# Kernel tuning notes

Hardware: AMD Instinct MI355X
Metric: run time of the kernel (lower is better)

## Reference

```python
import jax, jax.numpy as jnp
import numpy as np


def setup_inputs() -> dict:
    key = jax.random.key(0)
    R = 200  # num_regions (Schaefer-200 atlas scale)
    init_state = 0.1 * jax.random.normal(key, (R, 6), dtype=jnp.float32)
    # canonical Jansen-Rit parameters
    params = dict(A=3.25, a=100.0, B=22.0, b=50.0,
                  c1=135.0, c2=0.8 * 135.0, c3=0.25 * 135.0, c4=0.25 * 135.0,
                  vmax=5.0, v0=6.0, r=0.56, std_in=150.0)
    inp = {"init_state": init_state,
           "step_size": jnp.float32(1e-4),
           "num_steps": 20000}
    for k, v in params.items():
        inp[k] = jnp.float32(v)
    return inp


def reference(init_state, step_size, A, a, B, b, c1, c2, c3, c4,
              vmax, v0, r, std_in, num_steps):
    # sigmoid(x) = vmax / (1 + exp(r*(v0 - x)))
    def sig(x):
        return vmax / (1.0 + jnp.exp(r * (v0 - x)))

    dt = step_size

    def step(carry, _):
        M, E, I, Mv, Ev, Iv = carry  # each [R]
        dMv = A * a * sig(E - I) - 2.0 * a * Mv - M * a ** 2
        dEv = A * a * (std_in + c2 * sig(c1 * M)) - 2.0 * a * Ev - E * a ** 2
        dIv = B * b * (c4 * sig(c3 * M)) - 2.0 * b * Iv - I * b ** 2
        new = (M + dt * Mv, E + dt * Ev, I + dt * Iv,
               Mv + dt * dMv, Ev + dt * dEv, Iv + dt * dIv)
        return new, jnp.stack(new, axis=1)  # [R, 6] per-step history

    init = tuple(init_state[:, i] for i in range(6))
    final, state_hist = jax.lax.scan(step, init, None, length=num_steps)
    state_vals = jnp.stack(final, axis=1)  # [R, 6]
    return state_vals, state_hist  # ([R,6], [num_steps, R, 6])
```

## Files before the change

kernel.cpp:

```cpp
#include <hip/hip_runtime.h>


#define RLOG2E 1.44269504088896340736f

__global__ __launch_bounds__(64)
void jansen_kernel(const float* __restrict__ init_state,
                   const float* __restrict__ p_dt,
                   const int*   __restrict__ p_nsteps,
                   const float* __restrict__ pA,    const float* __restrict__ pa,
                   const float* __restrict__ pB,    const float* __restrict__ pb,
                   const float* __restrict__ pc1,   const float* __restrict__ pc2,
                   const float* __restrict__ pc3,   const float* __restrict__ pc4,
                   const float* __restrict__ pvmax, const float* __restrict__ pv0,
                   const float* __restrict__ pr,    const float* __restrict__ pstd,
                   float* __restrict__ out, int R)
{
    const int reg = blockIdx.x * 64 + threadIdx.x;
    if (reg >= R) return;

    const float dt     = *p_dt;
    const int   nsteps = *p_nsteps;
    const float A = *pA, a = *pa, B = *pB, b = *pb;
    const float c1 = *pc1, c2 = *pc2, c3 = *pc3, c4 = *pc4;
    const float vmax = *pvmax, v0 = *pv0, rsl = *pr, std_in = *pstd;

    const float cl2 = rsl * RLOG2E;
    const float cv0 = cl2 * v0;
    const float nE  = -cl2;
    const float nM1 = -cl2 * c1;
    const float nM3 = -cl2 * c3;

    const float kMv = 1.0f - 2.0f * a * dt;
    const float kIv = 1.0f - 2.0f * b * dt;
    const float kM  = -dt * a * a;
    const float kI  = -dt * b * b;
    const float kSE  = dt * A * a * vmax;
    const float kSM1 = dt * A * a * c2 * vmax;
    const float kSM3 = dt * B * b * c4 * vmax;
    const float kIn  = dt * A * a * std_in;

    float M  = init_state[reg * 6 + 0];
    float E  = init_state[reg * 6 + 1];
    float I  = init_state[reg * 6 + 2];
    float Mv = init_state[reg * 6 + 3];
    float Ev = init_state[reg * 6 + 4];
    float Iv = init_state[reg * 6 + 5];

    const int R6 = R * 6;
    float* hist = out + R6 + (size_t)reg * 6;

    #define STEP()                                                              \
    do {                                                                        \
        float eE  = __builtin_amdgcn_exp2f(fmaf(nE,  E - I, cv0));              \
        float eM1 = __builtin_amdgcn_exp2f(fmaf(nM1, M,     cv0));              \
        float eM3 = __builtin_amdgcn_exp2f(fmaf(nM3, M,     cv0));              \
        float rE  = __builtin_amdgcn_rcpf(1.0f + eE);                           \
        float rM1 = __builtin_amdgcn_rcpf(1.0f + eM1);                          \
        float rM3 = __builtin_amdgcn_rcpf(1.0f + eM3);                          \
        float nMv_ = fmaf(kMv, Mv, fmaf(kSE,  rE,  kM * M));                    \
        float nEv_ = fmaf(kMv, Ev, fmaf(kSM1, rM1, fmaf(kM, E, kIn)));          \
        float nIv_ = fmaf(kIv, Iv, fmaf(kSM3, rM3, kI * I));                    \
        float nM_  = fmaf(dt, Mv, M);                                           \
        float nE_  = fmaf(dt, Ev, E);                                           \
        float nI_  = fmaf(dt, Iv, I);                                           \
        M = nM_; E = nE_; I = nI_; Mv = nMv_; Ev = nEv_; Iv = nIv_;             \
        ((float2*)hist)[0] = make_float2(M, E);                                 \
        ((float2*)hist)[1] = make_float2(I, Mv);                                \
        ((float2*)hist)[2] = make_float2(Ev, Iv);                               \
        hist += R6;                                                             \
    } while (0)

    const int UN = 16;
    int s = 0;
    for (; s + UN <= nsteps; s += UN) {
        #pragma unroll
        for (int u = 0; u < UN; ++u) {
            STEP();
        }
    }
    for (; s < nsteps; ++s) {
        STEP();
    }
    #undef STEP

    float* fin = out + reg * 6;
    ((float2*)fin)[0] = make_float2(M, E);
    ((float2*)fin)[1] = make_float2(I, Mv);
    ((float2*)fin)[2] = make_float2(Ev, Iv);
}

extern "C" void kernel_launch(void* const* d_in, const int* in_sizes, int n_in,
                              void* d_out, int out_size, void* d_ws, size_t ws_size,
                              hipStream_t stream)
{
    const float* init = (const float*)d_in[0];
    const float* dt   = (const float*)d_in[1];
    const int*   ns   = (const int*)d_in[2];
    const int R = in_sizes[0] / 6;

    dim3 grid((R + 63) / 64), block(64);
    jansen_kernel<<<grid, block, 0, stream>>>(
        init, dt, ns,
        (const float*)d_in[3],  (const float*)d_in[4],
        (const float*)d_in[5],  (const float*)d_in[6],
        (const float*)d_in[7],  (const float*)d_in[8],
        (const float*)d_in[9],  (const float*)d_in[10],
        (const float*)d_in[11], (const float*)d_in[12],
        (const float*)d_in[13], (const float*)d_in[14],
        (float*)d_out, R);
}
```

Before: 1.474 ms.

## Stage per-step history in LDS and write coalesced chunks to global

Each thread now writes its state for 16 steps into shared memory, and after a barrier the whole block copies those rows to global memory in coalesced float2 writes. The old code issued strided per-thread writes with a 24-byte stride. The aim is to cut the cost of inefficient global store transactions on the 20000-step serial recurrence. In exchange it adds two barriers per chunk plus extra LDS traffic on the latency-bound serial path.

```diff
diff --git a/kernel.cpp b/kernel.cpp
--- a/kernel.cpp
+++ b/kernel.cpp
@@ -2,6 +2,7 @@
 
 
 #define RLOG2E 1.44269504088896340736f
+#define KC 16
 
 __global__ __launch_bounds__(64)
 void jansen_kernel(const float* __restrict__ init_state,
@@ -15,8 +16,12 @@
                    const float* __restrict__ pr,    const float* __restrict__ pstd,
                    float* __restrict__ out, int R)
 {
-    const int reg = blockIdx.x * 64 + threadIdx.x;
-    if (reg >= R) return;
+    __shared__ float lds[KC * 64 * 6];
+
+    const int lane = threadIdx.x;
+    const int blk  = blockIdx.x;
+    const int reg  = blk * 64 + lane;
+    const int lreg = (reg < R) ? reg : (R - 1);
 
     const float dt     = *p_dt;
     const int   nsteps = *p_nsteps;
@@ -39,17 +44,19 @@
     const float kSM3 = dt * B * b * c4 * vmax;
     const float kIn  = dt * A * a * std_in;
 
-    float M  = init_state[reg * 6 + 0];
-    float E  = init_state[reg * 6 + 1];
-    float I  = init_state[reg * 6 + 2];
-    float Mv = init_state[reg * 6 + 3];
-    float Ev = init_state[reg * 6 + 4];
-    float Iv = init_state[reg * 6 + 5];
+    float M  = init_state[lreg * 6 + 0];
+    float E  = init_state[lreg * 6 + 1];
+    float I  = init_state[lreg * 6 + 2];
+    float Mv = init_state[lreg * 6 + 3];
+    float Ev = init_state[lreg * 6 + 4];
+    float Iv = init_state[lreg * 6 + 5];
 
-    const int R6 = R * 6;
-    float* hist = out + R6 + (size_t)reg * 6;
+    const int R6   = R * 6;
+    const int nact = min(64, R - blk * 64);
+    const int S    = nact * 6;
+    float* rowBase = out + R6 + (size_t)blk * 64 * 6;
 
-    #define STEP()                                                              \
+    #define STEP(u)                                                             \
     do {                                                                        \
         float eE  = __builtin_amdgcn_exp2f(fmaf(nE,  E - I, cv0));              \
         float eM1 = __builtin_amdgcn_exp2f(fmaf(nM1, M,     cv0));              \
@@ -64,29 +71,65 @@
         float nE_  = fmaf(dt, Ev, E);                                           \
         float nI_  = fmaf(dt, Iv, I);                                           \
         M = nM_; E = nE_; I = nI_; Mv = nMv_; Ev = nEv_; Iv = nIv_;             \
-        ((float2*)hist)[0] = make_float2(M, E);                                 \
-        ((float2*)hist)[1] = make_float2(I, Mv);                                \
-        ((float2*)hist)[2] = make_float2(Ev, Iv);                               \
-        hist += R6;                                                             \
+        float* l = lds + (u) * 384 + lane * 6;                                  \
+        ((float2*)l)[0] = make_float2(M, E);                                    \
+        ((float2*)l)[1] = make_float2(I, Mv);                                   \
+        ((float2*)l)[2] = make_float2(Ev, Iv);                                  \
     } while (0)
 
-    const int UN = 16;
-    int s = 0;
-    for (; s + UN <= nsteps; s += UN) {
+    const int nchunks = nsteps / KC;
+    for (int c = 0; c < nchunks; ++c) {
         #pragma unroll
-        for (int u = 0; u < UN; ++u) {
-            STEP();
+        for (int u = 0; u < KC; ++u) {
+            STEP(u);
         }
+        __syncthreads();
+
+        float* rb = rowBase + (size_t)(c * KC) * R6;
+        if (S == 384) {
+            #pragma unroll
+            for (int u = 0; u < KC; ++u) {
+                const float* l = lds + u * 384;
+                float*       g = rb + (size_t)u * R6;
+                #pragma unroll
+                for (int p = 0; p < 3; ++p) {
+                    int d = p * 128 + 2 * lane;
+                    *(float2*)(g + d) = *(const float2*)(l + d);
+                }
+            }
+        } else {
+            #pragma unroll
+            for (int u = 0; u < KC; ++u) {
+                const float* l = lds + u * 384;
+                float*       g = rb + (size_t)u * R6;
+                #pragma unroll
+                for (int p = 0; p < 3; ++p) {
+                    int d = p * 128 + 2 * lane;
+                    if (d < S) *(float2*)(g + d) = *(const float2*)(l + d);
+                }
+            }
+        }
+        __syncthreads();
     }
-    for (; s < nsteps; ++s) {
-        STEP();
+
+    for (int s = nchunks * KC; s < nsteps; ++s) {
+        STEP(0);
+        if (reg < R) {
+            float* g = out + R6 + (size_t)s * R6 + (size_t)reg * 6;
+            const float* l = lds + lane * 6;
+            ((float2*)g)[0] = ((const float2*)l)[0];
+            ((float2*)g)[1] = ((const float2*)l)[1];
+            ((float2*)g)[2] = ((const float2*)l)[2];
+        }
     }
     #undef STEP
 
-    float* fin = out + reg * 6;
-    ((float2*)fin)[0] = make_float2(M, E);
-    ((float2*)fin)[1] = make_float2(I, Mv);
-    ((float2*)fin)[2] = make_float2(Ev, Iv);
+    if (reg < R) {
+        float* fin = out + (size_t)reg * 6;
+        ((float2*)fin)[0] = make_float2(M, E);
+        ((float2*)fin)[1] = make_float2(I, Mv);
+        ((float2*)fin)[2] = make_float2(Ev, Iv);
+    }
 }
 
 extern "C" void kernel_launch(void* const* d_in, const int* in_sizes, int n_in,
```

Result: slower. 2.805 ms (+90.4%).
